# Optimization experiments

Hardware: AMD Instinct MI355X
Metric: run time of the kernel (lower is better)

Reference implementation:

```python
import jax, jax.numpy as jnp
import numpy as np

N, E = 50000, 250000          # nodes, edges
IN, OUT, EDIM = 9, 84, 1      # NNConv(9, 84), edge nn Linear(1, 9*84)
EPS = 1e-5                    # BatchNorm1d default eps


def setup_inputs() -> dict:
    key = jax.random.key(0)
    ks = jax.random.split(key, 8)
    return {
        "x": jax.random.normal(ks[0], (N, IN), jnp.float32),
        "edge_index": jax.random.randint(ks[1], (2, E), 0, N, dtype=jnp.int64),
        "edge_attr": jax.random.normal(ks[2], (E, EDIM), jnp.float32),
        # edge nn: Linear(EDIM, IN*OUT) generating per-edge weight matrices
        "nn_w": jax.random.normal(ks[3], (EDIM, IN * OUT), jnp.float32) * (1.0 / np.sqrt(EDIM)),
        "nn_b": jnp.zeros((IN * OUT,), jnp.float32),
        # NNConv root weight + bias
        "root": jax.random.normal(ks[4], (IN, OUT), jnp.float32) * (1.0 / np.sqrt(IN)),
        "bias": jnp.zeros((OUT,), jnp.float32),
        # BatchNorm1d(84) affine params
        "gamma": jnp.ones((OUT,), jnp.float32),
        "beta": jnp.zeros((OUT,), jnp.float32),
    }


def reference(x, edge_index, edge_attr, nn_w, nn_b, root, bias, gamma, beta):
    src, dst = edge_index[0], edge_index[1]
    # per-edge weight matrices: [E, IN, OUT]
    w_e = (edge_attr @ nn_w + nn_b).reshape(E, IN, OUT)
    # gather source node features and apply edge-specific matmul: [E, OUT]
    msg = jnp.einsum('ei,eio->eo', x[src], w_e)
    # scatter-add to destination nodes (NNConv default aggr='add'): [N, OUT]
    aggr = jax.ops.segment_sum(msg, dst, num_segments=N)
    out = x @ root + aggr + bias
    # BatchNorm1d(84), training mode (biased batch stats)
    mean = out.mean(0)
    var = out.var(0)
    out = (out - mean) * jax.lax.rsqrt(var + EPS) * gamma + beta
    return out
```

## Files before the change

kernel.cpp:

```cpp
#include <hip/hip_runtime.h>

#define N_NODES 50000
#define E_EDGES 250000
#define IN_F 9
#define OUT_F 84
#define GROUPS 21
#define BN_EPS 1e-5f

#define NB_TILE 48
#define NTILES ((N_NODES + NB_TILE - 1) / NB_TILE)
#define NCOPIES 32
#define CAP 32

#define VDIM 27
#define NPAIR 378
#define NM 405
#define SLEN 408

#define CNT_OFF   0
#define STATC_OFF 50048
#define ZERO_WORDS 63104
#define SLOT_OFF  63232
#define S_OFF     3263232

__global__ void fill_slots_kernel(const int* __restrict__ ei,
                                  const float* __restrict__ ea,
                                  int* __restrict__ cnt,
                                  int2* __restrict__ slot) {
    int e = blockIdx.x * blockDim.x + threadIdx.x;
    if (e < E_EDGES) {
        int dst = ei[E_EDGES + e];
        int pos = atomicAdd(&cnt[dst], 1);
        if (pos < CAP)
            slot[dst * CAP + pos] = make_int2(ei[e], __float_as_int(ea[e]));
    }
}

__global__ void gather_gram_kernel(const float* __restrict__ x,
                                   const int*   __restrict__ cnt,
                                   const int2*  __restrict__ slot,
                                   float* __restrict__ S,
                                   float* __restrict__ statc) {
    __shared__ float V[VDIM * (NB_TILE + 1)];
    __shared__ __align__(16) int2 rec[NB_TILE][CAP];
    __shared__ int cnt_s[NB_TILE];
    __shared__ unsigned char pI[NPAIR], pJ[NPAIR];

    const int tid = threadIdx.x;
    const int nbase = blockIdx.x * NB_TILE;

    for (int t = tid; t < NPAIR; t += blockDim.x) {
        int tt = t, i = 0;
        while (tt >= VDIM - i) { tt -= VDIM - i; ++i; }
        pI[t] = (unsigned char)i;
        pJ[t] = (unsigned char)(i + tt);
    }
    if (tid < NB_TILE) {
        int n = nbase + tid;
        int c = (n < N_NODES) ? cnt[n] : 0;
        cnt_s[tid] = (c > CAP) ? CAP : c;
    }
    __syncthreads();

    if (tid < NB_TILE * 4) {
        int nl = tid >> 2, part = tid & 3;
        int c = cnt_s[nl];
        const int4* grow = (const int4*)&slot[(nbase + nl) * CAP];
        int4* lrow = (int4*)&rec[nl][0];
#pragma unroll
        for (int j = 0; j < 4; ++j) {
            int s = part * 8 + j * 2;
            if (s < c) lrow[part * 4 + j] = grow[part * 4 + j];
        }
    }
    __syncthreads();

    for (int it = tid; it < NB_TILE * IN_F; it += blockDim.x) {
        int nl = it / IN_F, i = it - nl * IN_F;
        int n = nbase + nl;
        float xv = 0.f, s0 = 0.f, s1 = 0.f;
        if (n < N_NODES) {
            xv = x[n * IN_F + i];
            int c = cnt_s[nl];
            const int2* r = rec[nl];
            int k = 0;
            for (; k + 4 <= c; k += 4) {
                int2 r0 = r[k], r1 = r[k+1], r2 = r[k+2], r3 = r[k+3];
                float a0 = x[r0.x * IN_F + i];
                float a1 = x[r1.x * IN_F + i];
                float a2 = x[r2.x * IN_F + i];
                float a3 = x[r3.x * IN_F + i];
                s0 += (a0 + a1) + (a2 + a3);
                s1 += __int_as_float(r0.y) * a0 + __int_as_float(r1.y) * a1
                    + __int_as_float(r2.y) * a2 + __int_as_float(r3.y) * a3;
            }
            for (; k < c; ++k) {
                int2 r0 = r[k];
                float a0 = x[r0.x * IN_F + i];
                s0 += a0;
                s1 += __int_as_float(r0.y) * a0;
            }
            S[n * 18 + i]     = s0;
            S[n * 18 + 9 + i] = s1;
        }
        V[i * (NB_TILE + 1) + nl]        = xv;
        V[(9 + i) * (NB_TILE + 1) + nl]  = s0;
        V[(18 + i) * (NB_TILE + 1) + nl] = s1;
    }
    __syncthreads();

    float* sc = statc + (blockIdx.x & (NCOPIES - 1)) * SLEN;
    for (int t = tid; t < NM; t += blockDim.x) {
        float acc = 0.f;
        if (t < NPAIR) {
            const float* vi = &V[pI[t] * (NB_TILE + 1)];
            const float* vj = &V[pJ[t] * (NB_TILE + 1)];
#pragma unroll
            for (int n = 0; n < NB_TILE; ++n) acc += vi[n] * vj[n];
        } else {
            const float* vi = &V[(t - NPAIR) * (NB_TILE + 1)];
#pragma unroll
            for (int n = 0; n < NB_TILE; ++n) acc += vi[n];
        }
        atomicAdd(&sc[t], acc);
    }
}

__global__ void final_kernel(const float* __restrict__ x,
                             const float* __restrict__ S,
                             const float* __restrict__ nw,
                             const float* __restrict__ nb,
                             const float* __restrict__ root,
                             const float* __restrict__ bias,
                             const float* __restrict__ gamma,
                             const float* __restrict__ beta,
                             const float* __restrict__ statc,
                             float* __restrict__ out) {
    __shared__ __align__(16) float4 Ws[IN_F * GROUPS];
    __shared__ __align__(16) float4 Bs[IN_F * GROUPS];
    __shared__ __align__(16) float4 Rs[IN_F * GROUPS];
    __shared__ __align__(16) float4 bs4[GROUPS];
    __shared__ float M[NM];
    __shared__ __align__(16) float scale[OUT_F];
    __shared__ __align__(16) float shift[OUT_F];
    __shared__ float Xt[NB_TILE * IN_F];
    __shared__ float St[NB_TILE * 18];

    const int tid = threadIdx.x;
    const int nbase = blockIdx.x * NB_TILE;

    for (int t = tid; t < IN_F * GROUPS; t += blockDim.x) {
        Ws[t] = ((const float4*)nw)[t];
        Bs[t] = ((const float4*)nb)[t];
        Rs[t] = ((const float4*)root)[t];
    }
    if (tid < GROUPS) bs4[tid] = ((const float4*)bias)[tid];

    for (int it = tid; it < NB_TILE * IN_F; it += blockDim.x) {
        int nl = it / IN_F, i = it - nl * IN_F;
        int n = nbase + nl;
        float xv = 0.f, s0 = 0.f, s1 = 0.f;
        if (n < N_NODES) {
            xv = x[n * IN_F + i];
            s0 = S[n * 18 + i];
            s1 = S[n * 18 + 9 + i];
        }
        Xt[nl * IN_F + i]   = xv;
        St[nl * 18 + i]     = s0;
        St[nl * 18 + 9 + i] = s1;
    }

    for (int t = tid; t < NM; t += blockDim.x) {
        float a = 0.f;
#pragma unroll
        for (int c = 0; c < NCOPIES; ++c) a += statc[c * SLEN + t];
        M[t] = a;
    }
    __syncthreads();

    if (tid < OUT_F) {
        const int o = tid, g4 = o >> 2, cm = o & 3;
        float c[VDIM];
#pragma unroll
        for (int i = 0; i < IN_F; ++i) {
            c[i]      = ((const float*)&Rs[i * GROUPS + g4])[cm];
            c[9 + i]  = ((const float*)&Bs[i * GROUPS + g4])[cm];
            c[18 + i] = ((const float*)&Ws[i * GROUPS + g4])[cm];
        }
        float sv = 0.f;
#pragma unroll
        for (int i = 0; i < VDIM; ++i) sv += M[NPAIR + i] * c[i];
        float q = 0.f;
        int t2 = 0;
        for (int i = 0; i < VDIM; ++i) {
            q += c[i] * c[i] * M[t2++];
            for (int j = i + 1; j < VDIM; ++j)
                q += 2.f * c[i] * c[j] * M[t2++];
        }
        const float b = ((const float*)&bs4[g4])[cm];
        const float inv_n = 1.0f / (float)N_NODES;
        float mean  = (sv + (float)N_NODES * b) * inv_n;
        float sumsq = q + 2.f * b * sv + (float)N_NODES * b * b;
        float var   = sumsq * inv_n - mean * mean;
        float sc    = rsqrtf(var + BN_EPS) * gamma[o];
        scale[o] = sc;
        shift[o] = beta[o] - mean * sc;
    }
    __syncthreads();

    const int g = tid % GROUPS;
    if (tid < 252) {
        float4 sc4 = *(const float4*)&scale[g * 4];
        float4 sh4 = *(const float4*)&shift[g * 4];
#pragma unroll
        for (int k = 0; k < 4; ++k) {
            int p  = tid + k * 252;
            int nl = p / GROUPS;
            int n  = nbase + nl;
            if (n < N_NODES) {
                float4 acc = bs4[g];
#pragma unroll
                for (int i = 0; i < IN_F; ++i) {
                    float xv = Xt[nl * IN_F + i];
                    float s0 = St[nl * 18 + i];
                    float s1 = St[nl * 18 + 9 + i];
                    float4 r = Rs[i * GROUPS + g];
                    float4 w = Ws[i * GROUPS + g];
                    float4 b = Bs[i * GROUPS + g];
                    acc.x += xv * r.x + s1 * w.x + s0 * b.x;
                    acc.y += xv * r.y + s1 * w.y + s0 * b.y;
                    acc.z += xv * r.z + s1 * w.z + s0 * b.z;
                    acc.w += xv * r.w + s1 * w.w + s0 * b.w;
                }
                acc.x = acc.x * sc4.x + sh4.x;
                acc.y = acc.y * sc4.y + sh4.y;
                acc.z = acc.z * sc4.z + sh4.z;
                acc.w = acc.w * sc4.w + sh4.w;
                *(float4*)&out[n * OUT_F + g * 4] = acc;
            }
        }
    }
}

extern "C" void kernel_launch(void* const* d_in, const int* in_sizes, int n_in,
                              void* d_out, int out_size, void* d_ws, size_t ws_size,
                              hipStream_t stream) {
    const float* x     = (const float*)d_in[0];
    const int*   ei    = (const int*)d_in[1];
    const float* ea    = (const float*)d_in[2];
    const float* nw    = (const float*)d_in[3];
    const float* nb    = (const float*)d_in[4];
    const float* root  = (const float*)d_in[5];
    const float* bias  = (const float*)d_in[6];
    const float* gamma = (const float*)d_in[7];
    const float* beta  = (const float*)d_in[8];
    float*       out   = (float*)d_out;

    float* wsf   = (float*)d_ws;
    int*   wsi   = (int*)d_ws;
    int*   cnt   = wsi + CNT_OFF;
    float* statc = wsf + STATC_OFF;
    int2*  slot  = (int2*)(wsi + SLOT_OFF);
    float* S     = wsf + S_OFF;

    hipMemsetAsync(wsi, 0, ZERO_WORDS * sizeof(int), stream);
    fill_slots_kernel<<<(E_EDGES + 255) / 256, 256, 0, stream>>>(ei, ea, cnt, slot);
    gather_gram_kernel<<<NTILES, 256, 0, stream>>>(x, cnt, slot, S, statc);
    final_kernel<<<NTILES, 256, 0, stream>>>(x, S, nw, nb, root, bias,
                                             gamma, beta, statc, out);
}
```

Baseline: 120.8 us.

## Vectorize edge fill, pair Gram dot products, hoist BN stats into scale kernel

Edge slot filling now handles four edges per thread with vector loads of indices and attributes. The Gram-matrix reduction in the gather kernel reads float4 vectors from a padded 52-stride layout and computes two dot products per thread. BatchNorm scale and shift are computed once in a new single-block kernel instead of redundantly in every final-kernel block. The final kernel also interleaves four nodes per thread to reuse weight loads. Costs are an extra kernel launch and a small serial single-block stage between gather and final.

```diff
diff --git a/kernel.cpp b/kernel.cpp
--- a/kernel.cpp
+++ b/kernel.cpp
@@ -16,23 +16,34 @@
 #define NPAIR 378
 #define NM 405
 #define SLEN 408
+#define VSTR 52
+#define NSLOT 196
 
 #define CNT_OFF   0
 #define STATC_OFF 50048
 #define ZERO_WORDS 63104
 #define SLOT_OFF  63232
 #define S_OFF     3263232
+#define SS_OFF    4163232
 
 __global__ void fill_slots_kernel(const int* __restrict__ ei,
                                   const float* __restrict__ ea,
                                   int* __restrict__ cnt,
                                   int2* __restrict__ slot) {
-    int e = blockIdx.x * blockDim.x + threadIdx.x;
+    int e = (blockIdx.x * blockDim.x + threadIdx.x) * 4;
     if (e < E_EDGES) {
-        int dst = ei[E_EDGES + e];
-        int pos = atomicAdd(&cnt[dst], 1);
-        if (pos < CAP)
-            slot[dst * CAP + pos] = make_int2(ei[e], __float_as_int(ea[e]));
+        int4   s4 = *(const int4*)&ei[e];
+        int4   d4 = *(const int4*)&ei[E_EDGES + e];
+        float4 a4 = *(const float4*)&ea[e];
+        int pos;
+        pos = atomicAdd(&cnt[d4.x], 1);
+        if (pos < CAP) slot[d4.x * CAP + pos] = make_int2(s4.x, __float_as_int(a4.x));
+        pos = atomicAdd(&cnt[d4.y], 1);
+        if (pos < CAP) slot[d4.y * CAP + pos] = make_int2(s4.y, __float_as_int(a4.y));
+        pos = atomicAdd(&cnt[d4.z], 1);
+        if (pos < CAP) slot[d4.z * CAP + pos] = make_int2(s4.z, __float_as_int(a4.z));
+        pos = atomicAdd(&cnt[d4.w], 1);
+        if (pos < CAP) slot[d4.w * CAP + pos] = make_int2(s4.w, __float_as_int(a4.w));
     }
 }
 
@@ -41,20 +52,22 @@
                                    const int2*  __restrict__ slot,
                                    float* __restrict__ S,
                                    float* __restrict__ statc) {
-    __shared__ float V[VDIM * (NB_TILE + 1)];
+    __shared__ __align__(16) float V[VDIM * VSTR];
     __shared__ __align__(16) int2 rec[NB_TILE][CAP];
     __shared__ int cnt_s[NB_TILE];
-    __shared__ unsigned char pI[NPAIR], pJ[NPAIR];
+    __shared__ unsigned char sI[NSLOT], sJ[NSLOT];
 
     const int tid = threadIdx.x;
     const int nbase = blockIdx.x * NB_TILE;
 
-    for (int t = tid; t < NPAIR; t += blockDim.x) {
+    for (int t = tid; t < NSLOT; t += blockDim.x) {
         int tt = t, i = 0;
-        while (tt >= VDIM - i) { tt -= VDIM - i; ++i; }
-        pI[t] = (unsigned char)i;
-        pJ[t] = (unsigned char)(i + tt);
-    }
+        while (tt >= ((VDIM - i + 1) >> 1)) { tt -= (VDIM - i + 1) >> 1; ++i; }
+        sI[t] = (unsigned char)i;
+        sJ[t] = (unsigned char)(i + 2 * tt);
+    }
+    for (int t = tid; t < VDIM * 4; t += blockDim.x)
+        V[(t >> 2) * VSTR + NB_TILE + (t & 3)] = 0.f;
     if (tid < NB_TILE) {
         int n = nbase + tid;
         int c = (n < N_NODES) ? cnt[n] : 0;
@@ -103,26 +116,88 @@
             S[n * 18 + i]     = s0;
             S[n * 18 + 9 + i] = s1;
         }
-        V[i * (NB_TILE + 1) + nl]        = xv;
-        V[(9 + i) * (NB_TILE + 1) + nl]  = s0;
-        V[(18 + i) * (NB_TILE + 1) + nl] = s1;
+        V[i * VSTR + nl]        = xv;
+        V[(9 + i) * VSTR + nl]  = s0;
+        V[(18 + i) * VSTR + nl] = s1;
     }
     __syncthreads();
 
     float* sc = statc + (blockIdx.x & (NCOPIES - 1)) * SLEN;
+    for (int t = tid; t < NSLOT + VDIM; t += blockDim.x) {
+        if (t < NSLOT) {
+            int i = sI[t], j0 = sJ[t];
+            int h2 = (j0 < VDIM - 1);
+            const float4* vi = (const float4*)&V[i * VSTR];
+            const float4* va = (const float4*)&V[j0 * VSTR];
+            const float4* vb = (const float4*)&V[(j0 + h2) * VSTR];
+            float acc0 = 0.f, acc1 = 0.f;
+#pragma unroll
+            for (int m = 0; m < VSTR / 4; ++m) {
+                float4 a = vi[m], p = va[m], q = vb[m];
+                acc0 += a.x * p.x + a.y * p.y + a.z * p.z + a.w * p.w;
+                acc1 += a.x * q.x + a.y * q.y + a.z * q.z + a.w * q.w;
+            }
+            int base = i * VDIM - (i * (i - 1)) / 2;
+            atomicAdd(&sc[base + (j0 - i)], acc0);
+            if (h2) atomicAdd(&sc[base + (j0 - i) + 1], acc1);
+        } else {
+            int r = t - NSLOT;
+            const float4* vi = (const float4*)&V[r * VSTR];
+            float acc = 0.f;
+#pragma unroll
+            for (int m = 0; m < VSTR / 4; ++m) {
+                float4 a = vi[m];
+                acc += (a.x + a.y) + (a.z + a.w);
+            }
+            atomicAdd(&sc[NPAIR + r], acc);
+        }
+    }
+}
+
+__global__ void scale_kernel(const float* __restrict__ nw,
+                             const float* __restrict__ nb,
+                             const float* __restrict__ root,
+                             const float* __restrict__ bias,
+                             const float* __restrict__ gamma,
+                             const float* __restrict__ beta,
+                             const float* __restrict__ statc,
+                             float* __restrict__ ss) {
+    __shared__ float M[NM];
+    const int tid = threadIdx.x;
     for (int t = tid; t < NM; t += blockDim.x) {
-        float acc = 0.f;
-        if (t < NPAIR) {
-            const float* vi = &V[pI[t] * (NB_TILE + 1)];
-            const float* vj = &V[pJ[t] * (NB_TILE + 1)];
-#pragma unroll
-            for (int n = 0; n < NB_TILE; ++n) acc += vi[n] * vj[n];
-        } else {
-            const float* vi = &V[(t - NPAIR) * (NB_TILE + 1)];
-#pragma unroll
-            for (int n = 0; n < NB_TILE; ++n) acc += vi[n];
-        }
-        atomicAdd(&sc[t], acc);
+        float a = 0.f;
+#pragma unroll
+        for (int c = 0; c < NCOPIES; ++c) a += statc[c * SLEN + t];
+        M[t] = a;
+    }
+    __syncthreads();
+    if (tid < OUT_F) {
+        const int o = tid;
+        float c[VDIM];
+#pragma unroll
+        for (int i = 0; i < IN_F; ++i) {
+            c[i]      = root[i * OUT_F + o];
+            c[9 + i]  = nb[i * OUT_F + o];
+            c[18 + i] = nw[i * OUT_F + o];
+        }
+        float sv = 0.f;
+#pragma unroll
+        for (int i = 0; i < VDIM; ++i) sv += M[NPAIR + i] * c[i];
+        float q = 0.f;
+        int t2 = 0;
+        for (int i = 0; i < VDIM; ++i) {
+            q += c[i] * c[i] * M[t2++];
+            for (int j = i + 1; j < VDIM; ++j)
+                q += 2.f * c[i] * c[j] * M[t2++];
+        }
+        const float b = bias[o];
+        const float inv_n = 1.0f / (float)N_NODES;
+        float mean  = (sv + (float)N_NODES * b) * inv_n;
+        float sumsq = q + 2.f * b * sv + (float)N_NODES * b * b;
+        float var   = sumsq * inv_n - mean * mean;
+        float scl   = rsqrtf(var + BN_EPS) * gamma[o];
+        ss[o]         = scl;
+        ss[OUT_F + o] = beta[o] - mean * scl;
     }
 }
 
@@ -132,17 +207,13 @@
                              const float* __restrict__ nb,
                              const float* __restrict__ root,
                              const float* __restrict__ bias,
-                             const float* __restrict__ gamma,
-                             const float* __restrict__ beta,
-                             const float* __restrict__ statc,
+                             const float* __restrict__ ss,
                              float* __restrict__ out) {
     __shared__ __align__(16) float4 Ws[IN_F * GROUPS];
     __shared__ __align__(16) float4 Bs[IN_F * GROUPS];
     __shared__ __align__(16) float4 Rs[IN_F * GROUPS];
     __shared__ __align__(16) float4 bs4[GROUPS];
-    __shared__ float M[NM];
-    __shared__ __align__(16) float scale[OUT_F];
-    __shared__ __align__(16) float shift[OUT_F];
+    __shared__ __align__(16) float ssl[2 * OUT_F];
     __shared__ float Xt[NB_TILE * IN_F];
     __shared__ float St[NB_TILE * 18];
 
@@ -155,6 +226,7 @@
         Rs[t] = ((const float4*)root)[t];
     }
     if (tid < GROUPS) bs4[tid] = ((const float4*)bias)[tid];
+    if (tid < 2 * OUT_F) ssl[tid] = ss[tid];
 
     for (int it = tid; it < NB_TILE * IN_F; it += blockDim.x) {
         int nl = it / IN_F, i = it - nl * IN_F;
@@ -169,74 +241,46 @@
         St[nl * 18 + i]     = s0;
         St[nl * 18 + 9 + i] = s1;
     }
-
-    for (int t = tid; t < NM; t += blockDim.x) {
-        float a = 0.f;
-#pragma unroll
-        for (int c = 0; c < NCOPIES; ++c) a += statc[c * SLEN + t];
-        M[t] = a;
-    }
-    __syncthreads();
-
-    if (tid < OUT_F) {
-        const int o = tid, g4 = o >> 2, cm = o & 3;
-        float c[VDIM];
-#pragma unroll
-        for (int i = 0; i < IN_F; ++i) {
-            c[i]      = ((const float*)&Rs[i * GROUPS + g4])[cm];
-            c[9 + i]  = ((const float*)&Bs[i * GROUPS + g4])[cm];
-            c[18 + i] = ((const float*)&Ws[i * GROUPS + g4])[cm];
-        }
-        float sv = 0.f;
-#pragma unroll
-        for (int i = 0; i < VDIM; ++i) sv += M[NPAIR + i] * c[i];
-        float q = 0.f;
-        int t2 = 0;
-        for (int i = 0; i < VDIM; ++i) {
-            q += c[i] * c[i] * M[t2++];
-            for (int j = i + 1; j < VDIM; ++j)
-                q += 2.f * c[i] * c[j] * M[t2++];
-        }
-        const float b = ((const float*)&bs4[g4])[cm];
-        const float inv_n = 1.0f / (float)N_NODES;
-        float mean  = (sv + (float)N_NODES * b) * inv_n;
-        float sumsq = q + 2.f * b * sv + (float)N_NODES * b * b;
-        float var   = sumsq * inv_n - mean * mean;
-        float sc    = rsqrtf(var + BN_EPS) * gamma[o];
-        scale[o] = sc;
-        shift[o] = beta[o] - mean * sc;
-    }
     __syncthreads();
 
     const int g = tid % GROUPS;
     if (tid < 252) {
-        float4 sc4 = *(const float4*)&scale[g * 4];
-        float4 sh4 = *(const float4*)&shift[g * 4];
+        int nl[4];
+        float4 acc[4];
 #pragma unroll
         for (int k = 0; k < 4; ++k) {
-            int p  = tid + k * 252;
-            int nl = p / GROUPS;
-            int n  = nbase + nl;
+            int p = tid + k * 252;
+            nl[k] = p / GROUPS;
+            acc[k] = bs4[g];
+        }
+#pragma unroll
+        for (int i = 0; i < IN_F; ++i) {
+            float4 r = Rs[i * GROUPS + g];
+            float4 w = Ws[i * GROUPS + g];
+            float4 b = Bs[i * GROUPS + g];
+#pragma unroll
+            for (int k = 0; k < 4; ++k) {
+                float xv = Xt[nl[k] * IN_F + i];
+                float s0 = St[nl[k] * 18 + i];
+                float s1 = St[nl[k] * 18 + 9 + i];
+                acc[k].x += xv * r.x + s1 * w.x + s0 * b.x;
+                acc[k].y += xv * r.y + s1 * w.y + s0 * b.y;
+                acc[k].z += xv * r.z + s1 * w.z + s0 * b.z;
+                acc[k].w += xv * r.w + s1 * w.w + s0 * b.w;
+            }
+        }
+        float4 sc4 = *(const float4*)&ssl[g * 4];
+        float4 sh4 = *(const float4*)&ssl[OUT_F + g * 4];
+#pragma unroll
+        for (int k = 0; k < 4; ++k) {
+            int n = nbase + nl[k];
             if (n < N_NODES) {
-                float4 acc = bs4[g];
-#pragma unroll
-                for (int i = 0; i < IN_F; ++i) {
-                    float xv = Xt[nl * IN_F + i];
-                    float s0 = St[nl * 18 + i];
-                    float s1 = St[nl * 18 + 9 + i];
-                    float4 r = Rs[i * GROUPS + g];
-                    float4 w = Ws[i * GROUPS + g];
-                    float4 b = Bs[i * GROUPS + g];
-                    acc.x += xv * r.x + s1 * w.x + s0 * b.x;
-                    acc.y += xv * r.y + s1 * w.y + s0 * b.y;
-                    acc.z += xv * r.z + s1 * w.z + s0 * b.z;
-                    acc.w += xv * r.w + s1 * w.w + s0 * b.w;
-                }
-                acc.x = acc.x * sc4.x + sh4.x;
-                acc.y = acc.y * sc4.y + sh4.y;
-                acc.z = acc.z * sc4.z + sh4.z;
-                acc.w = acc.w * sc4.w + sh4.w;
-                *(float4*)&out[n * OUT_F + g * 4] = acc;
+                float4 a = acc[k];
+                a.x = a.x * sc4.x + sh4.x;
+                a.y = a.y * sc4.y + sh4.y;
+                a.z = a.z * sc4.z + sh4.z;
+                a.w = a.w * sc4.w + sh4.w;
+                *(float4*)&out[n * OUT_F + g * 4] = a;
             }
         }
     }
@@ -262,10 +306,11 @@
     float* statc = wsf + STATC_OFF;
     int2*  slot  = (int2*)(wsi + SLOT_OFF);
     float* S     = wsf + S_OFF;
+    float* ss    = wsf + SS_OFF;
 
     hipMemsetAsync(wsi, 0, ZERO_WORDS * sizeof(int), stream);
-    fill_slots_kernel<<<(E_EDGES + 255) / 256, 256, 0, stream>>>(ei, ea, cnt, slot);
+    fill_slots_kernel<<<(E_EDGES / 4 + 255) / 256, 256, 0, stream>>>(ei, ea, cnt, slot);
     gather_gram_kernel<<<NTILES, 256, 0, stream>>>(x, cnt, slot, S, statc);
-    final_kernel<<<NTILES, 256, 0, stream>>>(x, S, nw, nb, root, bias,
-                                             gamma, beta, statc, out);
-}
+    scale_kernel<<<1, 256, 0, stream>>>(nw, nb, root, bias, gamma, beta, statc, ss);
+    final_kernel<<<NTILES, 256, 0, stream>>>(x, S, nw, nb, root, bias, ss, out);
+}
```

Result: slower. 206.5 us (+70.9%).
